# Performance work log

Hardware: AMD Instinct MI355X
Metric: run time of the kernel (lower is better)

The kernel has to match this reference:

```python
import jax, jax.numpy as jnp
import numpy as np
import math

# dims: N batch, T seq, DM d_model, H heads, E caterpillar_height, L caterpillar_length
N, T, DM = 2, 2048, 1024
H, E, L = 8, 4, 32
DK, DV = 64, 64


def setup_inputs() -> dict:
    key = jax.random.key(0)
    ks = jax.random.split(key, 8)

    def randw(k, *d):
        return jax.random.normal(k, d, dtype=jnp.float32) / math.sqrt(d[-1])

    return {
        "X": jax.random.normal(ks[0], (N, T, DM), dtype=jnp.float32),
        "w_G": randw(ks[1], H, E, DM),
        "b_G": jnp.full((H, E), -math.log(E - 1), dtype=jnp.float32),
        "w_K": randw(ks[2], H, DK, DM),
        "w_V": randw(ks[3], H, DV, DM),
        "w_Q": randw(ks[4], H, DK, DM),
        "w_O": randw(ks[5], DV * H, DM),
        "init_K_rec": randw(ks[6], E, L, DK),
        "init_V_rec": randw(ks[7], E, L, DV),
    }


def _chunk_scan(A, Xg, Y_init):
    # recurrence over chunk axis (axis=2): Y[m] = A[m] * Y[m-1] + Xg[m]
    # A: (N,E,M,L,1), Xg: (N,E,M,L,d), Y_init: (N,E,L,d)
    def comb(c1, c2):
        a1, x1 = c1
        a2, x2 = c2
        return a1 * a2, a2 * x1 + x2

    Ab = jnp.broadcast_to(A, Xg.shape)
    Ac, Xc = jax.lax.associative_scan(comb, (Ab, Xg), axis=2)
    return Xc + Ac * Y_init[:, :, None, :, :]


def reference(X, w_G, b_G, w_K, w_V, w_Q, w_O, init_K_rec, init_V_rec):
    n, t, _ = X.shape
    h, e, _ = w_G.shape
    l = init_K_rec.shape[1]
    dk = w_K.shape[1]
    dv = w_V.shape[1]
    m = t // l  # number of chunks

    # gates and projections
    G = jax.nn.sigmoid(jnp.einsum("ntd,hed->nhet", X, w_G) + b_G[None, :, :, None])  # (n,h,e,t)
    V = jnp.einsum("ntc,hdc->nhtd", X, w_V)  # (n,h,t,dv)
    K = jnp.einsum("ntc,hdc->nhtd", X, w_K)  # (n,h,t,dk)
    A = 1.0 - G.sum(axis=1)  # (n,e,t)
    gated_K = jnp.einsum("nhet,nhtd->netd", G, K)  # (n,e,t,dk)
    gated_V = jnp.einsum("nhet,nhtd->netd", G, V)  # (n,e,t,dv)

    # chunk into (m, l) and run the linear recurrence over chunks
    A_c = A.reshape(n, e, m, l)[..., None]  # (n,e,m,l,1)
    init_K = jnp.broadcast_to(init_K_rec[None], (n, e, l, dk))
    init_V = jnp.broadcast_to(init_V_rec[None], (n, e, l, dv))
    next_K = _chunk_scan(A_c, gated_K.reshape(n, e, m, l, dk), init_K)
    next_V = _chunk_scan(A_c, gated_V.reshape(n, e, m, l, dv), init_V)

    # recurrent-state buffers: init states followed by scanned states -> length t + l
    rec_K = jnp.concatenate([init_K, next_K.reshape(n, e, t, dk)], axis=2)
    rec_V = jnp.concatenate([init_V, next_V.reshape(n, e, t, dv)], axis=2)

    # sliding windows of length l over the state buffer (torch as_strided moving_window)
    idx = jnp.arange(t)[:, None] + jnp.arange(l)[None, :]  # (t,l)
    buf_K = rec_K[:, :, 1:]  # (n,e,t+l-1,dk)
    buf_V = rec_V[:, :, 1:]
    uk = buf_K[:, :, idx]  # (n,e,t,l,dk)
    uv = buf_V[:, :, idx]  # (n,e,t,l,dv)

    Q = jnp.einsum("ntc,hdc->nhtd", X, w_Q)  # (n,h,t,dk)
    scores = jnp.einsum("nhtd,netld->nhtel", Q, uk) / math.sqrt(dk)  # (n,h,t,e,l)
    attn = jax.nn.softmax(scores.reshape(n, h, t, e * l), axis=3).reshape(scores.shape)
    Y = jnp.einsum("nhtel,netld->nthd", attn, uv).reshape(n, t, h * dv)
    return Y @ w_O
```

## Files before the change

### kernel.cpp

```cpp
#include <hip/hip_runtime.h>
#include <math.h>


typedef __attribute__((ext_vector_type(8))) short bf16x8;
typedef __attribute__((ext_vector_type(4))) float f32x4;

static __device__ __forceinline__ unsigned short f2bf(float f) {
  unsigned u = __float_as_uint(f);
  u += 0x7fffu + ((u >> 16) & 1u);
  return (unsigned short)(u >> 16);
}
static __device__ __forceinline__ float bf2f(unsigned short h) {
  return __uint_as_float(((unsigned)h) << 16);
}
static __device__ __forceinline__ unsigned packbf(float f) {
  unsigned short h = f2bf(f);
  unsigned short l = f2bf(f - bf2f(h));
  return ((unsigned)h << 16) | (unsigned)l;
}
static __device__ __forceinline__ float unpackbf(unsigned u) {
  return __uint_as_float(u & 0xffff0000u) + __uint_as_float(u << 16);
}

#define GLDS(gp, lp) \
  __builtin_amdgcn_global_load_lds((const __attribute__((address_space(1))) void*)(gp), \
                                   (__attribute__((address_space(3))) void*)(lp), 16, 0, 0)

__global__ __launch_bounds__(256) void cvt_X_split(const float* __restrict__ X,
                                                   unsigned short* __restrict__ Xh,
                                                   unsigned short* __restrict__ Xl) {
  const int i = (blockIdx.x * 256 + threadIdx.x) * 4;
  float4 v = *(const float4*)(X + i);
  ushort4 h, l;
  h.x = f2bf(v.x); l.x = f2bf(v.x - bf2f(h.x));
  h.y = f2bf(v.y); l.y = f2bf(v.y - bf2f(h.y));
  h.z = f2bf(v.z); l.z = f2bf(v.z - bf2f(h.z));
  h.w = f2bf(v.w); l.w = f2bf(v.w - bf2f(h.w));
  *(ushort4*)(Xh + i) = h;
  *(ushort4*)(Xl + i) = l;
}

__global__ __launch_bounds__(256) void cvt_W_split(const float* __restrict__ wK,
                                                   const float* __restrict__ wV,
                                                   const float* __restrict__ wQ,
                                                   const float* __restrict__ wG,
                                                   unsigned short* __restrict__ Wh,
                                                   unsigned short* __restrict__ Wl) {
  const int idx = (blockIdx.x * 256 + threadIdx.x) * 4;
  const int row = idx >> 10;
  const int col = idx & 1023;
  const float* src = nullptr;
  if (row < 512)       src = wK + (size_t)row * 1024;
  else if (row < 1024) src = wV + (size_t)(row - 512) * 1024;
  else if (row < 1536) src = wQ + (size_t)(row - 1024) * 1024;
  else if (row < 1568) src = wG + (size_t)(row - 1536) * 1024;
  float4 v = make_float4(0.f, 0.f, 0.f, 0.f);
  if (src) v = *(const float4*)(src + col);
  ushort4 h, l;
  h.x = f2bf(v.x); l.x = f2bf(v.x - bf2f(h.x));
  h.y = f2bf(v.y); l.y = f2bf(v.y - bf2f(h.y));
  h.z = f2bf(v.z); l.z = f2bf(v.z - bf2f(h.z));
  h.w = f2bf(v.w); l.w = f2bf(v.w - bf2f(h.w));
  *(ushort4*)(Wh + idx) = h;
  *(ushort4*)(Wl + idx) = l;
}

__global__ __launch_bounds__(256) void cvt_wOt_split(const float* __restrict__ wO,
                                                     unsigned short* __restrict__ wOth,
                                                     unsigned short* __restrict__ wOtl) {
  __shared__ float tile[32][33];
  const int tx = threadIdx.x;
  const int ty = threadIdx.y;
  const int n0 = blockIdx.x * 32;
  const int k0 = blockIdx.y * 32;
#pragma unroll
  for (int r = 0; r < 4; ++r)
    tile[ty * 4 + r][tx] = wO[(size_t)(k0 + ty * 4 + r) * 1024 + n0 + tx];
  __syncthreads();
#pragma unroll
  for (int r = 0; r < 4; ++r) {
    const float v = tile[tx][ty * 4 + r];
    const unsigned short h = f2bf(v);
    wOth[(size_t)(n0 + ty * 4 + r) * 512 + k0 + tx] = h;
    wOtl[(size_t)(n0 + ty * 4 + r) * 512 + k0 + tx] = f2bf(v - bf2f(h));
  }
}

__global__ __launch_bounds__(256) void gemm_proj(
    const unsigned short* __restrict__ Xh, const unsigned short* __restrict__ Xl,
    const unsigned short* __restrict__ Wh, const unsigned short* __restrict__ Wl,
    const float* __restrict__ bG,
    float* __restrict__ Kb, float* __restrict__ Vb, float* __restrict__ Qb,
    float* __restrict__ Gb)
{
  __shared__ __align__(16) unsigned short Ash[2 * 128 * 32];
  __shared__ __align__(16) unsigned short Asl[2 * 128 * 32];
  __shared__ __align__(16) unsigned short Bsh[2 * 128 * 32];
  __shared__ __align__(16) unsigned short Bsl[2 * 128 * 32];
  const int tid  = threadIdx.x;
  const int lane = tid & 63;
  const int w    = tid >> 6;
  const int wr   = w >> 1, wc = w & 1;
  const int lm   = lane & 15, lq = lane >> 4;
  const int rb   = blockIdx.x * 128;
  const int cb   = blockIdx.y * 128;
  const int srow = lane >> 2;
  const int skc  = (lane & 3) * 8;

  f32x4 acc[4][4] = {};
  for (int k0 = 0; k0 < 1024; k0 += 64) {
#pragma unroll
    for (int p = 0; p < 2; ++p)
#pragma unroll
      for (int c = 0; c < 2; ++c) {
        const int r0   = w * 32 + c * 16;
        const int ldso = (p * 128 + r0) * 32;
        const size_t ga = (size_t)(rb + r0 + srow) * 1024 + k0 + p * 32 + skc;
        const size_t gb = (size_t)(cb + r0 + srow) * 1024 + k0 + p * 32 + skc;
        GLDS(Xh + ga, Ash + ldso);
        GLDS(Xl + ga, Asl + ldso);
        GLDS(Wh + gb, Bsh + ldso);
        GLDS(Wl + gb, Bsl + ldso);
      }
    __syncthreads();
#pragma unroll
    for (int ks = 0; ks < 2; ++ks) {
      bf16x8 ah[4], al[4], bh[4], bl[4];
#pragma unroll
      for (int i = 0; i < 4; ++i) {
        const int off = (ks * 128 + wr * 64 + i * 16 + lm) * 32 + lq * 8;
        ah[i] = *(const bf16x8*)(Ash + off);
        al[i] = *(const bf16x8*)(Asl + off);
      }
#pragma unroll
      for (int j = 0; j < 4; ++j) {
        const int off = (ks * 128 + wc * 64 + j * 16 + lm) * 32 + lq * 8;
        bh[j] = *(const bf16x8*)(Bsh + off);
        bl[j] = *(const bf16x8*)(Bsl + off);
      }
#pragma unroll
      for (int i = 0; i < 4; ++i)
#pragma unroll
        for (int j = 0; j < 4; ++j) {
          acc[i][j] = __builtin_amdgcn_mfma_f32_16x16x32_bf16(ah[i], bh[j], acc[i][j], 0, 0, 0);
          acc[i][j] = __builtin_amdgcn_mfma_f32_16x16x32_bf16(ah[i], bl[j], acc[i][j], 0, 0, 0);
          acc[i][j] = __builtin_amdgcn_mfma_f32_16x16x32_bf16(al[i], bh[j], acc[i][j], 0, 0, 0);
        }
    }
    __syncthreads();
  }
#pragma unroll
  for (int i = 0; i < 4; ++i) {
#pragma unroll
    for (int j = 0; j < 4; ++j) {
      const int c = cb + wc * 64 + j * 16 + lm;
      if (c >= 1568) continue;
#pragma unroll
      for (int rr = 0; rr < 4; ++rr) {
        const int m = rb + wr * 64 + i * 16 + lq * 4 + rr;
        const int n = m >> 11, t = m & 2047;
        const float v = acc[i][j][rr];
        if (c < 512) {
          Kb[(size_t)((n * 8 + (c >> 6)) * 2048 + t) * 64 + (c & 63)] = v;
        } else if (c < 1024) {
          const int cc = c - 512;
          Vb[(size_t)((n * 8 + (cc >> 6)) * 2048 + t) * 64 + (cc & 63)] = v;
        } else if (c < 1536) {
          const int cc = c - 1024;
          Qb[(size_t)((n * 8 + (cc >> 6)) * 2048 + t) * 64 + (cc & 63)] = v;
        } else {
          const int cc = c - 1536;
          const float g = 1.0f / (1.0f + __expf(-(v + bG[cc])));
          Gb[(size_t)(n * 32 + cc) * 2048 + t] = g;
        }
      }
    }
  }
}

__global__ __launch_bounds__(256) void gate_combine(
    const float* __restrict__ Gb,
    const float* __restrict__ Kb,
    const float* __restrict__ Vb,
    float* __restrict__ Afac,
    unsigned* __restrict__ gK,
    unsigned* __restrict__ gV)
{
  const int d  = threadIdx.x & 63;
  const int e  = threadIdx.x >> 6;
  const int n  = blockIdx.x >> 8;
  const int t0 = (blockIdx.x & 255) * 8;
#pragma unroll
  for (int tt = 0; tt < 8; ++tt) {
    const int t = t0 + tt;
    float gk = 0.f, gv = 0.f, gs = 0.f;
#pragma unroll
    for (int h = 0; h < 8; ++h) {
      const float g = Gb[((size_t)(n * 32) + h * 4 + e) * 2048 + t];
      gs += g;
      gk = fmaf(g, Kb[(size_t)((n * 8 + h) * 2048 + t) * 64 + d], gk);
      gv = fmaf(g, Vb[(size_t)((n * 8 + h) * 2048 + t) * 64 + d], gv);
    }
    const size_t o = (size_t)((n * 4 + e) * 2048 + t) * 64 + d;
    gK[o] = packbf(gk);
    gV[o] = packbf(gv);
    if (d == 0) Afac[(size_t)(n * 4 + e) * 2048 + t] = 1.0f - gs;
  }
}

__global__ __launch_bounds__(64) void scan2(
    const float* __restrict__ Afac,
    const unsigned* __restrict__ gK,
    const unsigned* __restrict__ gV,
    const float* __restrict__ initK,
    const float* __restrict__ initV,
    unsigned* __restrict__ recK,
    unsigned* __restrict__ recV)
{
  const int d  = threadIdx.x;
  const int ne = blockIdx.x;
  const int i  = blockIdx.y;
  const int e  = ne & 3;
  const bool isV = (blockIdx.z != 0);
  const unsigned* src = (isV ? gV : gK) + ((size_t)ne * 2048 + i) * 64 + d;
  const float*   init = isV ? initV : initK;
  unsigned*       rec = isV ? recV : recK;

  float y = init[(size_t)(e * 32 + i) * 64 + d];
  rec[(size_t)(ne * 2080 + i) * 64 + d] = packbf(y);
  const float* Arow = Afac + (size_t)ne * 2048 + i;
  unsigned* dst = rec + ((size_t)ne * 2080 + 32 + i) * 64 + d;

  unsigned u0[8];
  float    a0[8];
#pragma unroll
  for (int k = 0; k < 8; ++k) {
    a0[k] = Arow[k * 32];
    u0[k] = src[(size_t)k * 2048];
  }
  for (int J = 0; J < 64; J += 8) {
    unsigned u1[8];
    float    a1[8];
    if (J + 8 < 64) {
#pragma unroll
      for (int k = 0; k < 8; ++k) {
        a1[k] = Arow[(J + 8 + k) * 32];
        u1[k] = src[(size_t)(J + 8 + k) * 2048];
      }
    }
#pragma unroll
    for (int k = 0; k < 8; ++k) {
      y = fmaf(a0[k], y, unpackbf(u0[k]));
      dst[(size_t)(J + k) * 2048] = packbf(y);
    }
#pragma unroll
    for (int k = 0; k < 8; ++k) { a0[k] = a1[k]; u0[k] = u1[k]; }
  }
}

#define TB 16
__global__ __launch_bounds__(512) void attn_kernel(
    const float* __restrict__ Qb,
    const unsigned* __restrict__ recK,
    const unsigned* __restrict__ recV,
    unsigned short* __restrict__ Ybh,
    unsigned short* __restrict__ Ybl)
{
  __shared__ __align__(16) unsigned short lds[32512];
  const int KS_HI = 0;
  const int KS_LO = 3456;
  const int VT_HI = 6912;
  const int VT_LO = 10496;
  const int PW0   = 14080;

  const int tid  = threadIdx.x;
  const int lane = tid & 63;
  const int w    = tid >> 6;
  const int lm   = lane & 15, lq = lane >> 4;
  const int n    = blockIdx.x >> 7;
  const int t0   = (blockIdx.x & 127) * TB;
  const int maxidx = (2078 - t0) * 64 + 63;

  bf16x8 aqh[2], aql[2];
  {
    const float* qrow = Qb + ((size_t)(n * 8 + w) * 2048 + t0 + lm) * 64 + lq * 8;
#pragma unroll
    for (int ks = 0; ks < 2; ++ks) {
      float4 q0 = *(const float4*)(qrow + ks * 32);
      float4 q1 = *(const float4*)(qrow + ks * 32 + 4);
      float qv[8] = {q0.x, q0.y, q0.z, q0.w, q1.x, q1.y, q1.z, q1.w};
#pragma unroll
      for (int j = 0; j < 8; ++j) {
        unsigned short h = f2bf(qv[j]);
        aqh[ks][j] = (short)h;
        aql[ks][j] = (short)f2bf(qv[j] - bf2f(h));
      }
    }
  }

  f32x4 S[4][3];
  for (int e = 0; e < 4; ++e) {
    __syncthreads();
    {
      const unsigned* src = recK + ((size_t)(n * 4 + e) * 2080 + t0 + 1) * 64;
#pragma unroll
      for (int p = 0; p < 6; ++p) {
        const int idx = tid + p * 512;
        const int sl = idx >> 6, d = idx & 63;
        const unsigned u = src[idx <= maxidx ? idx : maxidx];
        lds[KS_HI + sl * 72 + d] = (unsigned short)(u >> 16);
        lds[KS_LO + sl * 72 + d] = (unsigned short)(u & 0xffffu);
      }
    }
    __syncthreads();
#pragma unroll
    for (int j = 0; j < 3; ++j) {
      f32x4 s = {0.f, 0.f, 0.f, 0.f};
#pragma unroll
      for (int ks = 0; ks < 2; ++ks) {
        const int boff = (j * 16 + lm) * 72 + ks * 32 + lq * 8;
        bf16x8 bh = *(const bf16x8*)(lds + KS_HI + boff);
        bf16x8 bl = *(const bf16x8*)(lds + KS_LO + boff);
        s = __builtin_amdgcn_mfma_f32_16x16x32_bf16(aqh[ks], bh, s, 0, 0, 0);
        s = __builtin_amdgcn_mfma_f32_16x16x32_bf16(aqh[ks], bl, s, 0, 0, 0);
        s = __builtin_amdgcn_mfma_f32_16x16x32_bf16(aql[ks], bh, s, 0, 0, 0);
      }
      S[e][j] = s;
    }
  }

  const float NEG = -3.0e38f;
  float mx[4] = {NEG, NEG, NEG, NEG};
#pragma unroll
  for (int e = 0; e < 4; ++e)
#pragma unroll
    for (int j = 0; j < 3; ++j) {
      const int sl = j * 16 + lm;
#pragma unroll
      for (int rr = 0; rr < 4; ++rr) {
        const int m = lq * 4 + rr;
        const bool valid = ((unsigned)(sl - m) <= 31u);
        const float v = valid ? S[e][j][rr] * 0.125f : NEG;
        S[e][j][rr] = v;
        mx[rr] = fmaxf(mx[rr], v);
      }
    }
#pragma unroll
  for (int rr = 0; rr < 4; ++rr) {
    float m = mx[rr];
    m = fmaxf(m, __shfl_xor(m, 1));
    m = fmaxf(m, __shfl_xor(m, 2));
    m = fmaxf(m, __shfl_xor(m, 4));
    m = fmaxf(m, __shfl_xor(m, 8));
    mx[rr] = m;
  }
  float sm[4] = {0.f, 0.f, 0.f, 0.f};
#pragma unroll
  for (int e = 0; e < 4; ++e)
#pragma unroll
    for (int j = 0; j < 3; ++j)
#pragma unroll
      for (int rr = 0; rr < 4; ++rr) {
        const float p = __expf(S[e][j][rr] - mx[rr]);
        S[e][j][rr] = p;
        sm[rr] += p;
      }
  float inv[4];
#pragma unroll
  for (int rr = 0; rr < 4; ++rr) {
    float s = sm[rr];
    s += __shfl_xor(s, 1);
    s += __shfl_xor(s, 2);
    s += __shfl_xor(s, 4);
    s += __shfl_xor(s, 8);
    inv[rr] = 1.0f / s;
  }

  const int PWH = PW0 + w * 1152;
  const int PWL = PW0 + 9216 + w * 1152;
  {
    const int r = lane >> 2, c0 = 48 + (lane & 3) * 4;
#pragma unroll
    for (int c = 0; c < 4; ++c) {
      lds[PWH + r * 72 + c0 + c] = 0;
      lds[PWL + r * 72 + c0 + c] = 0;
    }
  }
  f32x4 O[4] = {};
  for (int e = 0; e < 4; ++e) {
    __syncthreads();
    {
      const unsigned* src = recV + ((size_t)(n * 4 + e) * 2080 + t0 + 1) * 64;
#pragma unroll
      for (int p = 0; p < 6; ++p) {
        const int idx = tid + p * 512;
        const int sl = idx >> 6, d = idx & 63;
        const unsigned u = src[idx <= maxidx ? idx : maxidx];
        lds[VT_HI + d * 56 + sl] = (unsigned short)(u >> 16);
        lds[VT_LO + d * 56 + sl] = (unsigned short)(u & 0xffffu);
      }
    }
#pragma unroll
    for (int j = 0; j < 3; ++j)
#pragma unroll
      for (int rr = 0; rr < 4; ++rr) {
        const float p = S[e][j][rr] * inv[rr];
        const unsigned short h = f2bf(p);
        lds[PWH + (lq * 4 + rr) * 72 + j * 16 + lm] = h;
        lds[PWL + (lq * 4 + rr) * 72 + j * 16 + lm] = f2bf(p - bf2f(h));
      }
    __syncthreads();
    bf16x8 ah[2], al[2];
#pragma unroll
    for (int ks = 0; ks < 2; ++ks) {
      ah[ks] = *(const bf16x8*)(lds + PWH + lm * 72 + ks * 32 + lq * 8);
      al[ks] = *(const bf16x8*)(lds + PWL + lm * 72 + ks * 32 + lq * 8);
    }
#pragma unroll
    for (int nt = 0; nt < 4; ++nt)
#pragma unroll
      for (int ks = 0; ks < 2; ++ks) {
        const int boff = (nt * 16 + lm) * 56 + ks * 32 + lq * 8;
        bf16x8 vh = *(const bf16x8*)(lds + VT_HI + boff);
        bf16x8 vl = *(const bf16x8*)(lds + VT_LO + boff);
        O[nt] = __builtin_amdgcn_mfma_f32_16x16x32_bf16(ah[ks], vh, O[nt], 0, 0, 0);
        O[nt] = __builtin_amdgcn_mfma_f32_16x16x32_bf16(ah[ks], vl, O[nt], 0, 0, 0);
        O[nt] = __builtin_amdgcn_mfma_f32_16x16x32_bf16(al[ks], vh, O[nt], 0, 0, 0);
      }
  }

#pragma unroll
  for (int nt = 0; nt < 4; ++nt)
#pragma unroll
    for (int rr = 0; rr < 4; ++rr) {
      const int t = t0 + lq * 4 + rr;
      const size_t oi = ((size_t)(n * 2048 + t)) * 512 + w * 64 + nt * 16 + lm;
      const float v = O[nt][rr];
      const unsigned short h = f2bf(v);
      Ybh[oi] = h;
      Ybl[oi] = f2bf(v - bf2f(h));
    }
}

__global__ __launch_bounds__(256) void gemm_out(
    const unsigned short* __restrict__ Yh, const unsigned short* __restrict__ Yl,
    const unsigned short* __restrict__ Wh, const unsigned short* __restrict__ Wl,
    float* __restrict__ out)
{
  __shared__ __align__(16) unsigned short Ash[2 * 128 * 32];
  __shared__ __align__(16) unsigned short Asl[2 * 128 * 32];
  __shared__ __align__(16) unsigned short Bsh[2 * 128 * 32];
  __shared__ __align__(16) unsigned short Bsl[2 * 128 * 32];
  const int tid  = threadIdx.x;
  const int lane = tid & 63;
  const int w    = tid >> 6;
  const int wr   = w >> 1, wc = w & 1;
  const int lm   = lane & 15, lq = lane >> 4;
  const int rb   = blockIdx.x * 128;
  const int cb   = blockIdx.y * 128;
  const int srow = lane >> 2;
  const int skc  = (lane & 3) * 8;

  f32x4 acc[4][4] = {};
  for (int k0 = 0; k0 < 512; k0 += 64) {
#pragma unroll
    for (int p = 0; p < 2; ++p)
#pragma unroll
      for (int c = 0; c < 2; ++c) {
        const int r0   = w * 32 + c * 16;
        const int ldso = (p * 128 + r0) * 32;
        const size_t ga = (size_t)(rb + r0 + srow) * 512 + k0 + p * 32 + skc;
        const size_t gb = (size_t)(cb + r0 + srow) * 512 + k0 + p * 32 + skc;
        GLDS(Yh + ga, Ash + ldso);
        GLDS(Yl + ga, Asl + ldso);
        GLDS(Wh + gb, Bsh + ldso);
        GLDS(Wl + gb, Bsl + ldso);
      }
    __syncthreads();
#pragma unroll
    for (int ks = 0; ks < 2; ++ks) {
      bf16x8 ah[4], al[4], bh[4], bl[4];
#pragma unroll
      for (int i = 0; i < 4; ++i) {
        const int off = (ks * 128 + wr * 64 + i * 16 + lm) * 32 + lq * 8;
        ah[i] = *(const bf16x8*)(Ash + off);
        al[i] = *(const bf16x8*)(Asl + off);
      }
#pragma unroll
      for (int j = 0; j < 4; ++j) {
        const int off = (ks * 128 + wc * 64 + j * 16 + lm) * 32 + lq * 8;
        bh[j] = *(const bf16x8*)(Bsh + off);
        bl[j] = *(const bf16x8*)(Bsl + off);
      }
#pragma unroll
      for (int i = 0; i < 4; ++i)
#pragma unroll
        for (int j = 0; j < 4; ++j) {
          acc[i][j] = __builtin_amdgcn_mfma_f32_16x16x32_bf16(ah[i], bh[j], acc[i][j], 0, 0, 0);
          acc[i][j] = __builtin_amdgcn_mfma_f32_16x16x32_bf16(ah[i], bl[j], acc[i][j], 0, 0, 0);
          acc[i][j] = __builtin_amdgcn_mfma_f32_16x16x32_bf16(al[i], bh[j], acc[i][j], 0, 0, 0);
        }
    }
    __syncthreads();
  }
#pragma unroll
  for (int i = 0; i < 4; ++i)
#pragma unroll
    for (int j = 0; j < 4; ++j)
#pragma unroll
      for (int rr = 0; rr < 4; ++rr) {
        const int m = rb + wr * 64 + i * 16 + lq * 4 + rr;
        const int c = cb + wc * 64 + j * 16 + lm;
        out[(size_t)m * 1024 + c] = acc[i][j][rr];
      }
}

extern "C" void kernel_launch(void* const* d_in, const int* in_sizes, int n_in,
                              void* d_out, int out_size, void* d_ws, size_t ws_size,
                              hipStream_t stream) {
  const float* X     = (const float*)d_in[0];
  const float* wG    = (const float*)d_in[1];
  const float* bG    = (const float*)d_in[2];
  const float* wK    = (const float*)d_in[3];
  const float* wV    = (const float*)d_in[4];
  const float* wQ    = (const float*)d_in[5];
  const float* wO    = (const float*)d_in[6];
  const float* initK = (const float*)d_in[7];
  const float* initV = (const float*)d_in[8];
  float* out = (float*)d_out;

  float* ws = (float*)d_ws;
  float* Kb = ws;
  float* Vb = Kb + 2097152;
  float* Qb = Vb + 2097152;
  float* Gb = Qb + 2097152;
  unsigned short* Xh   = (unsigned short*)(Gb + 131072);
  unsigned short* Xl   = Xh + 4194304;
  unsigned short* Wh   = Xl + 4194304;
  unsigned short* Wl   = Wh + 1703936;
  unsigned short* wOth = Wl + 1703936;
  unsigned short* wOtl = wOth + 524288;
  unsigned* P    = (unsigned*)Xh;
  unsigned* recK = P;
  unsigned* recV = P + 1064960;
  unsigned* gK   = P + 2129920;
  unsigned* gV   = (unsigned*)Wh;
  float*   Afac  = (float*)(gV + 1048576);
  unsigned short* Ybh = (unsigned short*)Kb;
  unsigned short* Ybl = Ybh + 2097152;

  cvt_X_split<<<dim3(4096), dim3(256), 0, stream>>>(X, Xh, Xl);
  cvt_W_split<<<dim3(1664), dim3(256), 0, stream>>>(wK, wV, wQ, wG, Wh, Wl);
  cvt_wOt_split<<<dim3(32, 16), dim3(32, 8), 0, stream>>>(wO, wOth, wOtl);
  gemm_proj<<<dim3(32, 13), dim3(256), 0, stream>>>(Xh, Xl, Wh, Wl, bG, Kb, Vb, Qb, Gb);
  gate_combine<<<dim3(512), dim3(256), 0, stream>>>(Gb, Kb, Vb, Afac, gK, gV);
  scan2<<<dim3(8, 32, 2), dim3(64), 0, stream>>>(Afac, gK, gV, initK, initV, recK, recV);
  attn_kernel<<<dim3(256), dim3(512), 0, stream>>>(Qb, recK, recV, Ybh, Ybl);
  gemm_out<<<dim3(32, 8), dim3(256), 0, stream>>>(Ybh, Ybl, wOth, wOtl, out);
}
```

Baseline: 198.5 us.

## Merge conversion kernels, restructure gate_combine, preload all K/V into LDS in attention

Merges the X and W bf16-split conversion kernels into a single launch. gate_combine now stages gates in shared memory and reads each K/V element once for all four E outputs, instead of once per E. The attention kernel loads all four K and V state windows into a larger LDS buffer up front, which removes the per-E barriers. It also drops the low part of V, cutting one of the three MFMAs in the PV product. This lowers precision for V, and the larger LDS footprint may reduce occupancy.

```diff
diff --git a/kernel.cpp b/kernel.cpp
--- a/kernel.cpp
+++ b/kernel.cpp
@@ -26,43 +26,42 @@
   __builtin_amdgcn_global_load_lds((const __attribute__((address_space(1))) void*)(gp), \
                                    (__attribute__((address_space(3))) void*)(lp), 16, 0, 0)
 
-__global__ __launch_bounds__(256) void cvt_X_split(const float* __restrict__ X,
-                                                   unsigned short* __restrict__ Xh,
-                                                   unsigned short* __restrict__ Xl) {
-  const int i = (blockIdx.x * 256 + threadIdx.x) * 4;
-  float4 v = *(const float4*)(X + i);
+__global__ __launch_bounds__(256) void cvt_XW(
+    const float* __restrict__ X,
+    const float* __restrict__ wK, const float* __restrict__ wV,
+    const float* __restrict__ wQ, const float* __restrict__ wG,
+    unsigned short* __restrict__ Xh, unsigned short* __restrict__ Xl,
+    unsigned short* __restrict__ Wh, unsigned short* __restrict__ Wl)
+{
+  const int g = blockIdx.x * 256 + threadIdx.x;
+  const float* src;
+  unsigned short *dh, *dl;
+  int idx;
+  if (g < 1048576) {
+    idx = g * 4;
+    src = X + idx;
+    dh = Xh + idx; dl = Xl + idx;
+  } else {
+    idx = (g - 1048576) * 4;
+    const int row = idx >> 10;
+    const int col = idx & 1023;
+    const float* s = nullptr;
+    if (row < 512)       s = wK + (size_t)row * 1024;
+    else if (row < 1024) s = wV + (size_t)(row - 512) * 1024;
+    else if (row < 1536) s = wQ + (size_t)(row - 1024) * 1024;
+    else if (row < 1568) s = wG + (size_t)(row - 1536) * 1024;
+    src = s ? s + col : nullptr;
+    dh = Wh + idx; dl = Wl + idx;
+  }
+  float4 v = make_float4(0.f, 0.f, 0.f, 0.f);
+  if (src) v = *(const float4*)src;
   ushort4 h, l;
   h.x = f2bf(v.x); l.x = f2bf(v.x - bf2f(h.x));
   h.y = f2bf(v.y); l.y = f2bf(v.y - bf2f(h.y));
   h.z = f2bf(v.z); l.z = f2bf(v.z - bf2f(h.z));
   h.w = f2bf(v.w); l.w = f2bf(v.w - bf2f(h.w));
-  *(ushort4*)(Xh + i) = h;
-  *(ushort4*)(Xl + i) = l;
-}
-
-__global__ __launch_bounds__(256) void cvt_W_split(const float* __restrict__ wK,
-                                                   const float* __restrict__ wV,
-                                                   const float* __restrict__ wQ,
-                                                   const float* __restrict__ wG,
-                                                   unsigned short* __restrict__ Wh,
-                                                   unsigned short* __restrict__ Wl) {
-  const int idx = (blockIdx.x * 256 + threadIdx.x) * 4;
-  const int row = idx >> 10;
-  const int col = idx & 1023;
-  const float* src = nullptr;
-  if (row < 512)       src = wK + (size_t)row * 1024;
-  else if (row < 1024) src = wV + (size_t)(row - 512) * 1024;
-  else if (row < 1536) src = wQ + (size_t)(row - 1024) * 1024;
-  else if (row < 1568) src = wG + (size_t)(row - 1536) * 1024;
-  float4 v = make_float4(0.f, 0.f, 0.f, 0.f);
-  if (src) v = *(const float4*)(src + col);
-  ushort4 h, l;
-  h.x = f2bf(v.x); l.x = f2bf(v.x - bf2f(h.x));
-  h.y = f2bf(v.y); l.y = f2bf(v.y - bf2f(h.y));
-  h.z = f2bf(v.z); l.z = f2bf(v.z - bf2f(h.z));
-  h.w = f2bf(v.w); l.w = f2bf(v.w - bf2f(h.w));
-  *(ushort4*)(Wh + idx) = h;
-  *(ushort4*)(Wl + idx) = l;
+  *(ushort4*)dh = h;
+  *(ushort4*)dl = l;
 }
 
 __global__ __launch_bounds__(256) void cvt_wOt_split(const float* __restrict__ wO,
@@ -186,25 +185,46 @@
     unsigned* __restrict__ gK,
     unsigned* __restrict__ gV)
 {
-  const int d  = threadIdx.x & 63;
-  const int e  = threadIdx.x >> 6;
-  const int n  = blockIdx.x >> 8;
-  const int t0 = (blockIdx.x & 255) * 8;
-#pragma unroll
-  for (int tt = 0; tt < 8; ++tt) {
-    const int t = t0 + tt;
-    float gk = 0.f, gv = 0.f, gs = 0.f;
+  __shared__ float Gs[16][32];
+  const int tid = threadIdx.x;
+  const int n   = blockIdx.x >> 7;
+  const int t0  = (blockIdx.x & 127) * 16;
+  for (int idx = tid; idx < 512; idx += 256) {
+    const int he = idx & 31, tl = idx >> 5;
+    Gs[tl][he] = Gb[((size_t)n * 32 + he) * 2048 + t0 + tl];
+  }
+  __syncthreads();
+  const int d  = tid & 63;
+  const int ts = tid >> 6;
+#pragma unroll
+  for (int tt = 0; tt < 4; ++tt) {
+    const int tl = ts * 4 + tt;
+    const int t  = t0 + tl;
+    float ak[4] = {}, av[4] = {};
 #pragma unroll
     for (int h = 0; h < 8; ++h) {
-      const float g = Gb[((size_t)(n * 32) + h * 4 + e) * 2048 + t];
-      gs += g;
-      gk = fmaf(g, Kb[(size_t)((n * 8 + h) * 2048 + t) * 64 + d], gk);
-      gv = fmaf(g, Vb[(size_t)((n * 8 + h) * 2048 + t) * 64 + d], gv);
-    }
-    const size_t o = (size_t)((n * 4 + e) * 2048 + t) * 64 + d;
-    gK[o] = packbf(gk);
-    gV[o] = packbf(gv);
-    if (d == 0) Afac[(size_t)(n * 4 + e) * 2048 + t] = 1.0f - gs;
+      const float kk = Kb[(size_t)((n * 8 + h) * 2048 + t) * 64 + d];
+      const float vv = Vb[(size_t)((n * 8 + h) * 2048 + t) * 64 + d];
+#pragma unroll
+      for (int e = 0; e < 4; ++e) {
+        const float g = Gs[tl][h * 4 + e];
+        ak[e] = fmaf(g, kk, ak[e]);
+        av[e] = fmaf(g, vv, av[e]);
+      }
+    }
+#pragma unroll
+    for (int e = 0; e < 4; ++e) {
+      const size_t o = (size_t)((n * 4 + e) * 2048 + t) * 64 + d;
+      gK[o] = packbf(ak[e]);
+      gV[o] = packbf(av[e]);
+    }
+  }
+  if (tid < 64) {
+    const int e = tid & 3, tl = tid >> 2;
+    float gs = 0.f;
+#pragma unroll
+    for (int h = 0; h < 8; ++h) gs += Gs[tl][h * 4 + e];
+    Afac[(size_t)(n * 4 + e) * 2048 + t0 + tl] = 1.0f - gs;
   }
 }
 
@@ -259,6 +279,11 @@
 }
 
 #define TB 16
+#define KS_SZ 3456
+#define KS_LO 13824
+#define VT_B  27648
+#define VT_SZ 5120
+#define P_B   48128
 __global__ __launch_bounds__(512) void attn_kernel(
     const float* __restrict__ Qb,
     const unsigned* __restrict__ recK,
@@ -266,13 +291,7 @@
     unsigned short* __restrict__ Ybh,
     unsigned short* __restrict__ Ybl)
 {
-  __shared__ __align__(16) unsigned short lds[32512];
-  const int KS_HI = 0;
-  const int KS_LO = 3456;
-  const int VT_HI = 6912;
-  const int VT_LO = 10496;
-  const int PW0   = 14080;
-
+  __shared__ __align__(16) unsigned short lds[66560];
   const int tid  = threadIdx.x;
   const int lane = tid & 63;
   const int w    = tid >> 6;
@@ -298,36 +317,56 @@
     }
   }
 
+#pragma unroll
+  for (int e = 0; e < 4; ++e) {
+    const unsigned* sK = recK + ((size_t)(n * 4 + e) * 2080 + t0 + 1) * 64;
+    const unsigned* sV = recV + ((size_t)(n * 4 + e) * 2080 + t0 + 1) * 64;
+#pragma unroll
+    for (int p = 0; p < 6; ++p) {
+      const int idx = tid + p * 512;
+      const int ci  = idx <= maxidx ? idx : maxidx;
+      const int sl  = idx >> 6, d = idx & 63;
+      const unsigned uk = sK[ci];
+      const unsigned uv = sV[ci];
+      lds[e * KS_SZ + sl * 72 + d]         = (unsigned short)(uk >> 16);
+      lds[KS_LO + e * KS_SZ + sl * 72 + d] = (unsigned short)(uk & 0xffffu);
+      lds[VT_B + e * VT_SZ + d * 80 + sl]  = (unsigned short)(uv >> 16);
+    }
+  }
+  for (int idx = tid; idx < 2048; idx += 512) {
+    const int e = idx >> 9, r = idx & 511;
+    const int d = r >> 3, c = r & 7;
+    *(unsigned*)(lds + VT_B + e * VT_SZ + d * 80 + 48 + c * 2) = 0u;
+  }
+  const int PWH = P_B + w * 2304;
+  const int PWL = PWH + 1152;
+  {
+    const int r = lane >> 2, c0 = 48 + (lane & 3) * 4;
+#pragma unroll
+    for (int c = 0; c < 4; ++c) {
+      lds[PWH + r * 72 + c0 + c] = 0;
+      lds[PWL + r * 72 + c0 + c] = 0;
+    }
+  }
+  __syncthreads();
+
   f32x4 S[4][3];
-  for (int e = 0; e < 4; ++e) {
-    __syncthreads();
-    {
-      const unsigned* src = recK + ((size_t)(n * 4 + e) * 2080 + t0 + 1) * 64;
-#pragma unroll
-      for (int p = 0; p < 6; ++p) {
-        const int idx = tid + p * 512;
-        const int sl = idx >> 6, d = idx & 63;
-        const unsigned u = src[idx <= maxidx ? idx : maxidx];
-        lds[KS_HI + sl * 72 + d] = (unsigned short)(u >> 16);
-        lds[KS_LO + sl * 72 + d] = (unsigned short)(u & 0xffffu);
-      }
-    }
-    __syncthreads();
+#pragma unroll
+  for (int e = 0; e < 4; ++e)
 #pragma unroll
     for (int j = 0; j < 3; ++j) {
       f32x4 s = {0.f, 0.f, 0.f, 0.f};
 #pragma unroll
       for (int ks = 0; ks < 2; ++ks) {
         const int boff = (j * 16 + lm) * 72 + ks * 32 + lq * 8;
-        bf16x8 bh = *(const bf16x8*)(lds + KS_HI + boff);
-        bf16x8 bl = *(const bf16x8*)(lds + KS_LO + boff);
+        bf16x8 bh = *(const bf16x8*)(lds + e * KS_SZ + boff);
+        bf16x8 bl = *(const bf16x8*)(lds + KS_LO + e * KS_SZ + boff);
         s = __builtin_amdgcn_mfma_f32_16x16x32_bf16(aqh[ks], bh, s, 0, 0, 0);
         s = __builtin_amdgcn_mfma_f32_16x16x32_bf16(aqh[ks], bl, s, 0, 0, 0);
         s = __builtin_amdgcn_mfma_f32_16x16x32_bf16(aql[ks], bh, s, 0, 0, 0);
       }
       S[e][j] = s;
     }
-  }
 
   const float NEG = -3.0e38f;
   float mx[4] = {NEG, NEG, NEG, NEG};
@@ -376,30 +415,9 @@
     inv[rr] = 1.0f / s;
   }
 
-  const int PWH = PW0 + w * 1152;
-  const int PWL = PW0 + 9216 + w * 1152;
-  {
-    const int r = lane >> 2, c0 = 48 + (lane & 3) * 4;
-#pragma unroll
-    for (int c = 0; c < 4; ++c) {
-      lds[PWH + r * 72 + c0 + c] = 0;
-      lds[PWL + r * 72 + c0 + c] = 0;
-    }
-  }
   f32x4 O[4] = {};
+#pragma unroll
   for (int e = 0; e < 4; ++e) {
-    __syncthreads();
-    {
-      const unsigned* src = recV + ((size_t)(n * 4 + e) * 2080 + t0 + 1) * 64;
-#pragma unroll
-      for (int p = 0; p < 6; ++p) {
-        const int idx = tid + p * 512;
-        const int sl = idx >> 6, d = idx & 63;
-        const unsigned u = src[idx <= maxidx ? idx : maxidx];
-        lds[VT_HI + d * 56 + sl] = (unsigned short)(u >> 16);
-        lds[VT_LO + d * 56 + sl] = (unsigned short)(u & 0xffffu);
-      }
-    }
 #pragma unroll
     for (int j = 0; j < 3; ++j)
 #pragma unroll
@@ -409,7 +427,6 @@
         lds[PWH + (lq * 4 + rr) * 72 + j * 16 + lm] = h;
         lds[PWL + (lq * 4 + rr) * 72 + j * 16 + lm] = f2bf(p - bf2f(h));
       }
-    __syncthreads();
     bf16x8 ah[2], al[2];
 #pragma unroll
     for (int ks = 0; ks < 2; ++ks) {
@@ -420,11 +437,9 @@
     for (int nt = 0; nt < 4; ++nt)
 #pragma unroll
       for (int ks = 0; ks < 2; ++ks) {
-        const int boff = (nt * 16 + lm) * 56 + ks * 32 + lq * 8;
-        bf16x8 vh = *(const bf16x8*)(lds + VT_HI + boff);
-        bf16x8 vl = *(const bf16x8*)(lds + VT_LO + boff);
+        const int boff = (nt * 16 + lm) * 80 + ks * 32 + lq * 8;
+        bf16x8 vh = *(const bf16x8*)(lds + VT_B + e * VT_SZ + boff);
         O[nt] = __builtin_amdgcn_mfma_f32_16x16x32_bf16(ah[ks], vh, O[nt], 0, 0, 0);
-        O[nt] = __builtin_amdgcn_mfma_f32_16x16x32_bf16(ah[ks], vl, O[nt], 0, 0, 0);
         O[nt] = __builtin_amdgcn_mfma_f32_16x16x32_bf16(al[ks], vh, O[nt], 0, 0, 0);
       }
   }
@@ -549,11 +564,10 @@
   unsigned short* Ybh = (unsigned short*)Kb;
   unsigned short* Ybl = Ybh + 2097152;
 
-  cvt_X_split<<<dim3(4096), dim3(256), 0, stream>>>(X, Xh, Xl);
-  cvt_W_split<<<dim3(1664), dim3(256), 0, stream>>>(wK, wV, wQ, wG, Wh, Wl);
+  cvt_XW<<<dim3(5760), dim3(256), 0, stream>>>(X, wK, wV, wQ, wG, Xh, Xl, Wh, Wl);
   cvt_wOt_split<<<dim3(32, 16), dim3(32, 8), 0, stream>>>(wO, wOth, wOtl);
   gemm_proj<<<dim3(32, 13), dim3(256), 0, stream>>>(Xh, Xl, Wh, Wl, bG, Kb, Vb, Qb, Gb);
-  gate_combine<<<dim3(512), dim3(256), 0, stream>>>(Gb, Kb, Vb, Afac, gK, gV);
+  gate_combine<<<dim3(256), dim3(256), 0, stream>>>(Gb, Kb, Vb, Afac, gK, gV);
   scan2<<<dim3(8, 32, 2), dim3(64), 0, stream>>>(Afac, gK, gV, initK, initV, recK, recV);
   attn_kernel<<<dim3(256), dim3(512), 0, stream>>>(Qb, recK, recV, Ybh, Ybl);
   gemm_out<<<dim3(32, 8), dim3(256), 0, stream>>>(Ybh, Ybl, wOth, wOtl, out);
```

After: 193.2 us. 2.7% less time.
